# Kernel tuning notes

Measured on AMD Instinct MI355X. Metric: run time of the kernel, lower is better.

Reference implementation:

```python
import jax, jax.numpy as jnp
import numpy as np

B, C, S = 16, 128, 32          # batch, in_channel, img_size
HOLE_LO, HOLE_HI = 8, 24       # 16x16 hole where mask==1
HW = S * S
K = HW - (HOLE_HI - HOLE_LO) ** 2   # 768 context (unmasked) pixels per image
EPS = 1e-8                     # torch CosineSimilarity default eps


def setup_inputs() -> dict:
    key = jax.random.key(0)
    ks = jax.random.split(key, 3)
    x = jax.random.normal(ks[0], (B, C, S, S), dtype=jnp.float32)
    # mask: 1 inside the hole, 0 on the context region (fixed K per batch item)
    mask = jnp.zeros((B, 1, S, S), jnp.float32).at[:, :, HOLE_LO:HOLE_HI, HOLE_LO:HOLE_HI].set(1.0)
    # conv_regular_1: Conv2d(img_size**2 -> 256, k=5, pad=2); conv_regular_2: 256 -> 128
    W1 = jax.random.normal(ks[1], (256, HW, 5, 5), jnp.float32) / np.sqrt(HW * 25)
    b1 = jnp.zeros((256,), jnp.float32)
    W2 = jax.random.normal(ks[2], (128, 256, 5, 5), jnp.float32) / np.sqrt(256 * 25)
    b2 = jnp.zeros((128,), jnp.float32)
    return {"x": x, "mask": mask, "W1": W1, "b1": b1, "W2": W2, "b2": b2}


def _conv5x5(x, w, b):
    y = jax.lax.conv_general_dilated(x, w, window_strides=(1, 1),
                                     padding=[(2, 2), (2, 2)],
                                     dimension_numbers=("NCHW", "OIHW", "NCHW"))
    return y + b[None, :, None, None]


def reference(x, mask, W1, b1, W2, b2):
    # context (unmasked) pixel indices, row-major like torch.masked_select
    inv = (1.0 - mask[:, 0]) > 0.5                       # [B,S,S] bool
    idx = jax.vmap(lambda m: jnp.nonzero(m, size=K, fill_value=0)[0])(inv.reshape(B, HW))  # [B,K]
    xf = x.reshape(B, C, HW)                             # [B,C,HW]
    feat = jnp.take_along_axis(xf, idx[:, None, :], axis=2)  # [B,C,K] context features
    # cosine similarity over channel dim WITHOUT materializing [B,C,K,H,W] repeats
    dot = jnp.einsum("bck,bcp->bkp", feat, xf)           # [B,K,HW]
    nf = jnp.maximum(jnp.sqrt(jnp.sum(feat * feat, axis=1)), EPS)  # [B,K]
    nx = jnp.maximum(jnp.sqrt(jnp.sum(xf * xf, axis=1)), EPS)      # [B,HW]
    out = (dot / (nf[:, :, None] * nx[:, None, :])).reshape(B, K, S, S)
    out = out * mask                                     # keep hole region only
    pad = jnp.zeros((B, HW - K, S, S), out.dtype)
    out = jnp.concatenate([out, pad], axis=1)            # [B, HW, S, S]
    out = jax.nn.elu(_conv5x5(out, W1, b1))              # [B,256,S,S]
    out = jax.nn.elu(_conv5x5(out, W2, b2))              # [B,128,S,S]
    return out
```

## Files before the change

### kernel.cpp

```cpp
#include <hip/hip_runtime.h>
#include <hip/hip_fp16.h>
#include <math.h>


#define CC 128
#define HWN 1024
#define KK 768
#define PH 256

typedef _Float16 f16x8 __attribute__((ext_vector_type(8)));
typedef float f32x4 __attribute__((ext_vector_type(4)));

__device__ __forceinline__ int ctx_p(int k) {
    if (k < 256) return k;
    if (k < 512) {
        int r = (k - 256) >> 4, ci = (k - 256) & 15;
        int c = ci < 8 ? ci : ci + 16;
        return (8 + r) * 32 + c;
    }
    return k + 256;
}

__global__ __launch_bounds__(256) void kpre(const float* __restrict__ x,
                                            const float* __restrict__ W1, const float* __restrict__ W2,
                                            _Float16* __restrict__ cosT,
                                            _Float16* __restrict__ Wh1, _Float16* __restrict__ Wh2) {
    __shared__ float f[16][128];
    __shared__ float rfs[16];
    const int bid = blockIdx.x;
    const int t = threadIdx.x;
    if (bid < 768) {
        const int b = bid / 48;
        const int rem = bid - b * 48;
        const int hg = rem / 3, kch = rem - hg * 3;
        const int p16 = hg * 16;
        for (int s = t; s < 2048; s += 256) {
            int h = s >> 7, c = s & 127;
            int hp = p16 + h;
            f[h][c] = x[(b * CC + c) * HWN + (8 + (hp >> 4)) * 32 + 8 + (hp & 15)];
        }
        __syncthreads();
        {
            const int lane = t & 63, w = t >> 6;
#pragma unroll
            for (int i = 0; i < 4; ++i) {
                int h = w + i * 4;
                float v0 = f[h][lane], v1 = f[h][lane + 64];
                float pv = fmaf(v0, v0, v1 * v1);
#pragma unroll
                for (int m = 1; m < 64; m <<= 1) pv += __shfl_xor(pv, m, 64);
                if (lane == 0) rfs[h] = 1.0f / fmaxf(sqrtf(pv), 1e-8f);
            }
        }
        __syncthreads();
        const int k = kch * 256 + t;
        const int cp = ctx_p(k);
        const float* xp = x + b * CC * HWN + cp;
        float acc[16];
#pragma unroll
        for (int h = 0; h < 16; ++h) acc[h] = 0.f;
        float sk = 0.f;
        for (int c4 = 0; c4 < 128; c4 += 4) {
            float x0 = xp[(c4 + 0) * HWN];
            float x1 = xp[(c4 + 1) * HWN];
            float x2 = xp[(c4 + 2) * HWN];
            float x3 = xp[(c4 + 3) * HWN];
            sk = fmaf(x0, x0, sk); sk = fmaf(x1, x1, sk);
            sk = fmaf(x2, x2, sk); sk = fmaf(x3, x3, sk);
#pragma unroll
            for (int h = 0; h < 16; ++h) {
                float4 fv = *(const float4*)&f[h][c4];
                float a = acc[h];
                a = fmaf(fv.x, x0, a);
                a = fmaf(fv.y, x1, a);
                a = fmaf(fv.z, x2, a);
                a = fmaf(fv.w, x3, a);
                acc[h] = a;
            }
        }
        const float rk = 1.0f / fmaxf(sqrtf(sk), 1e-8f);
        _Float16* o = cosT + ((size_t)(b * PH + p16)) * KK + k;
#pragma unroll
        for (int h = 0; h < 16; ++h)
            o[(size_t)h * KK] = (_Float16)(acc[h] * rfs[h] * rk);
    } else {
        const int pid = bid - 768;
        if (pid < 768) {
            const int oc = pid & 255, kch = pid >> 8;
            const int k = kch * 256 + t;
            const float* wp = W1 + ((size_t)oc * HWN + k) * 25;
#pragma unroll
            for (int tap = 0; tap < 25; ++tap)
                Wh1[((size_t)(tap * 256 + oc)) * KK + k] = (_Float16)wp[tap];
        } else {
            const int oc = pid - 768;
            const float* wp = W2 + ((size_t)oc * 256 + t) * 25;
#pragma unroll
            for (int tap = 0; tap < 25; ++tap)
                Wh2[((size_t)(tap * 128 + oc)) * 256 + t] = (_Float16)wp[tap];
        }
    }
}

__global__ __launch_bounds__(512, 4) void kconv1m(const _Float16* __restrict__ cosT,
                                                  const _Float16* __restrict__ Wh1,
                                                  float* __restrict__ P, int kspan) {
    __shared__ __align__(16) char As[4 * 578 * 16];
    const int b = blockIdx.z, ks = blockIdx.x, nq = blockIdx.y;
    const int t = threadIdx.x;
    const int lane = t & 63, wid = t >> 6;
    const int mg = wid >> 1, ng = wid & 1;
    const int lm = lane & 15, kslot = lane >> 4;
    const int tile0 = (mg == 0) ? 0 : 6 * mg + 1;
    int pb[7];
#pragma unroll
    for (int mi = 0; mi < 7; ++mi) {
        int p = (tile0 + mi) * 16 + lm;
        if (p > 399) p = 399;
        pb[mi] = (kslot * 578 + (p / 20) * 24 + (p % 20)) * 16;
    }
    const f32x4 zero = {0.f, 0.f, 0.f, 0.f};
    f32x4 acc[7][2];
#pragma unroll
    for (int mi = 0; mi < 7; ++mi) { acc[mi][0] = zero; acc[mi][1] = zero; }

    const _Float16* Wb = Wh1 + (size_t)(nq * 64 + ng * 32 + lm) * KK + kslot * 8;

    const int kbeg = ks * kspan;
    for (int kc = kbeg; kc < kbeg + kspan; kc += 32) {
        __syncthreads();
        for (int s = t; s < 2304; s += 512) {
            int pos = s >> 2, slot = s & 3;
            int pu = pos / 24, pv = pos - pu * 24;
            int4 val = {0, 0, 0, 0};
            if (pu >= 4 && pu < 20 && pv >= 4 && pv < 20) {
                int hp = (pu - 4) * 16 + (pv - 4);
                val = *(const int4*)(cosT + ((size_t)(b * PH + hp)) * KK + kc + slot * 8);
            }
            *(int4*)(As + (slot * 578 + pos) * 16) = val;
        }
        __syncthreads();
        const _Float16* wkc = Wb + kc;
        f16x8 nb0 = *(const f16x8*)(wkc);
        f16x8 nb1 = *(const f16x8*)(wkc + 16 * KK);
#pragma unroll
        for (int tap = 0; tap < 25; ++tap) {
            const f16x8 b0 = nb0, b1 = nb1;
            if (tap < 24) {
                const _Float16* wn = wkc + (size_t)(tap + 1) * (256 * KK);
                nb0 = *(const f16x8*)(wn);
                nb1 = *(const f16x8*)(wn + 16 * KK);
            }
            const int off = ((tap / 5) * 24 + (tap % 5)) * 16;
#pragma unroll
            for (int mi = 0; mi < 6; ++mi) {
                f16x8 af = *(const f16x8*)(As + pb[mi] + off);
                acc[mi][0] = __builtin_amdgcn_mfma_f32_16x16x32_f16(af, b0, acc[mi][0], 0, 0, 0);
                acc[mi][1] = __builtin_amdgcn_mfma_f32_16x16x32_f16(af, b1, acc[mi][1], 0, 0, 0);
            }
            if (mg == 0) {
                f16x8 af = *(const f16x8*)(As + pb[6] + off);
                acc[6][0] = __builtin_amdgcn_mfma_f32_16x16x32_f16(af, b0, acc[6][0], 0, 0, 0);
                acc[6][1] = __builtin_amdgcn_mfma_f32_16x16x32_f16(af, b1, acc[6][1], 0, 0, 0);
            }
        }
    }
    float* Ps = P + ((size_t)((ks * 16 + b) * 4 + nq)) * 25600;
#pragma unroll
    for (int mi = 0; mi < 7; ++mi) {
        if (mi == 6 && mg != 0) continue;
#pragma unroll
        for (int j = 0; j < 2; ++j)
#pragma unroll
            for (int r = 0; r < 4; ++r) {
                int p = (tile0 + mi) * 16 + kslot * 4 + r;
                Ps[p * 64 + ng * 32 + j * 16 + lm] = acc[mi][j][r];
            }
    }
}

__global__ __launch_bounds__(256) void kreduce1(const float* __restrict__ P, const float* __restrict__ b1,
                                                _Float16* __restrict__ Y1T, int nks) {
    int i = blockIdx.x * 256 + threadIdx.x;
    int oc = i & 255;
    int nq = oc >> 6, ocl = oc & 63;
    int bp = i >> 8;
    int p = bp % 400, b = bp / 400;
    float s = 0.f;
    for (int ks = 0; ks < nks; ++ks)
        s += P[((size_t)((ks * 16 + b) * 4 + nq)) * 25600 + p * 64 + ocl];
    float y = s + b1[oc];
    y = y > 0.f ? y : expm1f(y);
    Y1T[((size_t)(b * 400 + p)) * 256 + oc] = (_Float16)y;
}

__global__ __launch_bounds__(512) void kconv2m(const _Float16* __restrict__ Y1T,
                                               const _Float16* __restrict__ Wh2,
                                               float* __restrict__ P) {
    __shared__ __align__(16) char As[4 * 786 * 16];
    const int b = blockIdx.z, ks = blockIdx.x, mh = blockIdx.y;
    const int t = threadIdx.x;
    const int lane = t & 63, wid = t >> 6;
    const int mg = wid >> 2, ng = wid & 3;
    const int lm = lane & 15, kslot = lane >> 4;
    const int ic0 = ks * 32;
    for (int s = t; s < 3136; s += 512) {
        int pos = s >> 2, slot = s & 3;
        int r = pos / 28, c = pos - r * 28;
        int4 val = {0, 0, 0, 0};
        if (r >= 4 && r < 24 && c >= 4 && c < 24)
            val = *(const int4*)(Y1T + ((size_t)(b * 400 + (r - 4) * 20 + (c - 4))) * 256 + ic0 + slot * 8);
        *(int4*)(As + (slot * 786 + pos) * 16) = val;
    }
    const int tile0 = mh * 18 + mg * 9;
    int pb[9];
#pragma unroll
    for (int mi = 0; mi < 9; ++mi) {
        int p = (tile0 + mi) * 16 + lm;
        pb[mi] = (kslot * 786 + (p / 24) * 28 + (p % 24)) * 16;
    }
    const f32x4 zero = {0.f, 0.f, 0.f, 0.f};
    f32x4 acc[9][2];
#pragma unroll
    for (int mi = 0; mi < 9; ++mi) { acc[mi][0] = zero; acc[mi][1] = zero; }
    const _Float16* Wb = Wh2 + (size_t)(ng * 32 + lm) * 256 + ic0 + kslot * 8;
    __syncthreads();
    f16x8 nb0 = *(const f16x8*)(Wb);
    f16x8 nb1 = *(const f16x8*)(Wb + 16 * 256);
#pragma unroll
    for (int tap = 0; tap < 25; ++tap) {
        const f16x8 b0 = nb0, b1 = nb1;
        if (tap < 24) {
            const _Float16* wn = Wb + (size_t)(tap + 1) * (128 * 256);
            nb0 = *(const f16x8*)(wn);
            nb1 = *(const f16x8*)(wn + 16 * 256);
        }
        const int off = ((tap / 5) * 28 + (tap % 5)) * 16;
#pragma unroll
        for (int mi = 0; mi < 9; ++mi) {
            f16x8 af = *(const f16x8*)(As + pb[mi] + off);
            acc[mi][0] = __builtin_amdgcn_mfma_f32_16x16x32_f16(af, b0, acc[mi][0], 0, 0, 0);
            acc[mi][1] = __builtin_amdgcn_mfma_f32_16x16x32_f16(af, b1, acc[mi][1], 0, 0, 0);
        }
    }
    float* Ps = P + ((size_t)((ks * 16 + b) * 2 + mh)) * 36864;
#pragma unroll
    for (int mi = 0; mi < 9; ++mi)
#pragma unroll
        for (int j = 0; j < 2; ++j)
#pragma unroll
            for (int r = 0; r < 4; ++r) {
                int p = (mg * 9 + mi) * 16 + kslot * 4 + r;
                Ps[p * 128 + ng * 32 + j * 16 + lm] = acc[mi][j][r];
            }
}

__global__ __launch_bounds__(256) void kreduce2(const float* __restrict__ P, const float* __restrict__ b2,
                                                float* __restrict__ out) {
    int i = blockIdx.x * 256 + threadIdx.x;
    int p = i & 1023;
    int oc = (i >> 10) & 127;
    int b = i >> 17;
    int u = p >> 5, v = p & 31;
    float y = 0.f;
    if (u >= 4 && u < 28 && v >= 4 && v < 28) {
        int pl = (u - 4) * 24 + (v - 4);
        int mh = pl >= 288 ? 1 : 0;
        int pll = pl - mh * 288;
        float s = 0.f;
#pragma unroll
        for (int ks = 0; ks < 8; ++ks)
            s += P[((size_t)((ks * 16 + b) * 2 + mh)) * 36864 + pll * 128 + oc];
        y = s + b2[oc];
        y = y > 0.f ? y : expm1f(y);
    }
    out[i] = y;
}

extern "C" void kernel_launch(void* const* d_in, const int* in_sizes, int n_in,
                              void* d_out, int out_size, void* d_ws, size_t ws_size,
                              hipStream_t stream) {
    const float* x  = (const float*)d_in[0];
    const float* W1 = (const float*)d_in[2];
    const float* b1 = (const float*)d_in[3];
    const float* W2 = (const float*)d_in[4];
    const float* b2 = (const float*)d_in[5];
    float* out = (float*)d_out;

    char* ws = (char*)d_ws;
    _Float16* cosT = (_Float16*)(ws + 0);
    _Float16* Wh1  = (_Float16*)(ws + 6291456);
    _Float16* Wh2  = (_Float16*)(ws + 16121856);
    _Float16* Y1T  = (_Float16*)(ws + 17760256);
    float*    P    = (float*)(ws + 21037056);

    const int nks = (ws_size >= 73465856ULL) ? 8 : 4;
    const int kspan = 768 / nks;

    kpre<<<1664, 256, 0, stream>>>(x, W1, W2, cosT, Wh1, Wh2);
    kconv1m<<<dim3(nks, 4, 16), 512, 0, stream>>>(cosT, Wh1, P, kspan);
    kreduce1<<<6400, 256, 0, stream>>>(P, b1, Y1T, nks);
    kconv2m<<<dim3(8, 2, 16), 512, 0, stream>>>(Y1T, Wh2, P);
    kreduce2<<<8192, 256, 0, stream>>>(P, b2, out);
}
```

Before: 271.0 us.

## Software-pipeline LDS and weight loads in conv MFMA loops; enlarge kpre tile

Both conv kernels now use double-buffered A fragments from LDS and triple-buffered B weight fragments from global memory, prefetching one or two taps ahead so MFMA issue overlaps load latency. The cosine-similarity precompute now handles 32 hole pixels per block instead of 16, which halves the number of times each context column of x is reread and changes the LDS load order. The cost is higher register pressure, with 32 accumulators in kpre and extra fragment buffers in the conv kernels, which could lower occupancy or cause spills under launch_bounds(512,4).

```diff
diff --git a/kernel.cpp b/kernel.cpp
--- a/kernel.cpp
+++ b/kernel.cpp
@@ -25,25 +25,25 @@
                                             const float* __restrict__ W1, const float* __restrict__ W2,
                                             _Float16* __restrict__ cosT,
                                             _Float16* __restrict__ Wh1, _Float16* __restrict__ Wh2) {
-    __shared__ float f[16][128];
-    __shared__ float rfs[16];
+    __shared__ float f[32][128];
+    __shared__ float rfs[32];
     const int bid = blockIdx.x;
     const int t = threadIdx.x;
-    if (bid < 768) {
-        const int b = bid / 48;
-        const int rem = bid - b * 48;
+    if (bid < 384) {
+        const int b = bid / 24;
+        const int rem = bid - b * 24;
         const int hg = rem / 3, kch = rem - hg * 3;
-        const int p16 = hg * 16;
-        for (int s = t; s < 2048; s += 256) {
-            int h = s >> 7, c = s & 127;
-            int hp = p16 + h;
+        const int p32 = hg * 32;
+        for (int s = t; s < 4096; s += 256) {
+            int h = s & 31, c = s >> 5;
+            int hp = p32 + h;
             f[h][c] = x[(b * CC + c) * HWN + (8 + (hp >> 4)) * 32 + 8 + (hp & 15)];
         }
         __syncthreads();
         {
             const int lane = t & 63, w = t >> 6;
 #pragma unroll
-            for (int i = 0; i < 4; ++i) {
+            for (int i = 0; i < 8; ++i) {
                 int h = w + i * 4;
                 float v0 = f[h][lane], v1 = f[h][lane + 64];
                 float pv = fmaf(v0, v0, v1 * v1);
@@ -56,9 +56,9 @@
         const int k = kch * 256 + t;
         const int cp = ctx_p(k);
         const float* xp = x + b * CC * HWN + cp;
-        float acc[16];
-#pragma unroll
-        for (int h = 0; h < 16; ++h) acc[h] = 0.f;
+        float acc[32];
+#pragma unroll
+        for (int h = 0; h < 32; ++h) acc[h] = 0.f;
         float sk = 0.f;
         for (int c4 = 0; c4 < 128; c4 += 4) {
             float x0 = xp[(c4 + 0) * HWN];
@@ -68,7 +68,7 @@
             sk = fmaf(x0, x0, sk); sk = fmaf(x1, x1, sk);
             sk = fmaf(x2, x2, sk); sk = fmaf(x3, x3, sk);
 #pragma unroll
-            for (int h = 0; h < 16; ++h) {
+            for (int h = 0; h < 32; ++h) {
                 float4 fv = *(const float4*)&f[h][c4];
                 float a = acc[h];
                 a = fmaf(fv.x, x0, a);
@@ -79,12 +79,12 @@
             }
         }
         const float rk = 1.0f / fmaxf(sqrtf(sk), 1e-8f);
-        _Float16* o = cosT + ((size_t)(b * PH + p16)) * KK + k;
-#pragma unroll
-        for (int h = 0; h < 16; ++h)
+        _Float16* o = cosT + ((size_t)(b * PH + p32)) * KK + k;
+#pragma unroll
+        for (int h = 0; h < 32; ++h)
             o[(size_t)h * KK] = (_Float16)(acc[h] * rfs[h] * rk);
     } else {
-        const int pid = bid - 768;
+        const int pid = bid - 384;
         if (pid < 768) {
             const int oc = pid & 255, kch = pid >> 8;
             const int k = kch * 256 + t;
@@ -101,6 +101,30 @@
         }
     }
 }
+
+#define LDA1(buf, tp) {                                                                   \
+        const int off_ = (((tp) / 5) * 24 + ((tp) % 5)) * 16;                             \
+        _Pragma("unroll")                                                                 \
+        for (int mi_ = 0; mi_ < 6; ++mi_)                                                 \
+            (buf)[mi_] = *(const f16x8*)(As + pb[mi_] + off_);                            \
+        if (mg == 0) (buf)[6] = *(const f16x8*)(As + pb[6] + off_);                       \
+    }
+#define LDB1(slot, tp) {                                                                  \
+        const _Float16* wn_ = wkc + (size_t)(tp) * (256 * KK);                            \
+        (slot)[0] = *(const f16x8*)(wn_);                                                 \
+        (slot)[1] = *(const f16x8*)(wn_ + 16 * KK);                                       \
+    }
+#define FMA1(buf, bb) {                                                                   \
+        _Pragma("unroll")                                                                 \
+        for (int mi_ = 0; mi_ < 6; ++mi_) {                                               \
+            acc[mi_][0] = __builtin_amdgcn_mfma_f32_16x16x32_f16((buf)[mi_], (bb)[0], acc[mi_][0], 0, 0, 0); \
+            acc[mi_][1] = __builtin_amdgcn_mfma_f32_16x16x32_f16((buf)[mi_], (bb)[1], acc[mi_][1], 0, 0, 0); \
+        }                                                                                 \
+        if (mg == 0) {                                                                    \
+            acc[6][0] = __builtin_amdgcn_mfma_f32_16x16x32_f16((buf)[6], (bb)[0], acc[6][0], 0, 0, 0); \
+            acc[6][1] = __builtin_amdgcn_mfma_f32_16x16x32_f16((buf)[6], (bb)[1], acc[6][1], 0, 0, 0); \
+        }                                                                                 \
+    }
 
 __global__ __launch_bounds__(512, 4) void kconv1m(const _Float16* __restrict__ cosT,
                                                   const _Float16* __restrict__ Wh1,
@@ -141,28 +165,16 @@
         }
         __syncthreads();
         const _Float16* wkc = Wb + kc;
-        f16x8 nb0 = *(const f16x8*)(wkc);
-        f16x8 nb1 = *(const f16x8*)(wkc + 16 * KK);
-#pragma unroll
-        for (int tap = 0; tap < 25; ++tap) {
-            const f16x8 b0 = nb0, b1 = nb1;
-            if (tap < 24) {
-                const _Float16* wn = wkc + (size_t)(tap + 1) * (256 * KK);
-                nb0 = *(const f16x8*)(wn);
-                nb1 = *(const f16x8*)(wn + 16 * KK);
-            }
-            const int off = ((tap / 5) * 24 + (tap % 5)) * 16;
-#pragma unroll
-            for (int mi = 0; mi < 6; ++mi) {
-                f16x8 af = *(const f16x8*)(As + pb[mi] + off);
-                acc[mi][0] = __builtin_amdgcn_mfma_f32_16x16x32_f16(af, b0, acc[mi][0], 0, 0, 0);
-                acc[mi][1] = __builtin_amdgcn_mfma_f32_16x16x32_f16(af, b1, acc[mi][1], 0, 0, 0);
-            }
-            if (mg == 0) {
-                f16x8 af = *(const f16x8*)(As + pb[6] + off);
-                acc[6][0] = __builtin_amdgcn_mfma_f32_16x16x32_f16(af, b0, acc[6][0], 0, 0, 0);
-                acc[6][1] = __builtin_amdgcn_mfma_f32_16x16x32_f16(af, b1, acc[6][1], 0, 0, 0);
-            }
+        f16x8 afq[2][7];
+        f16x8 bq[3][2];
+        LDA1(afq[0], 0);
+        LDB1(bq[0], 0);
+        LDB1(bq[1], 1);
+#pragma unroll
+        for (int tp = 0; tp < 25; ++tp) {
+            if (tp < 24) LDA1(afq[(tp + 1) & 1], tp + 1);
+            if (tp < 23) LDB1(bq[(tp + 2) % 3], tp + 2);
+            FMA1(afq[tp & 1], bq[tp % 3]);
         }
     }
     float* Ps = P + ((size_t)((ks * 16 + b) * 4 + nq)) * 25600;
@@ -193,6 +205,25 @@
     y = y > 0.f ? y : expm1f(y);
     Y1T[((size_t)(b * 400 + p)) * 256 + oc] = (_Float16)y;
 }
+
+#define LDA2(buf, tp) {                                                                   \
+        const int off_ = (((tp) / 5) * 28 + ((tp) % 5)) * 16;                             \
+        _Pragma("unroll")                                                                 \
+        for (int mi_ = 0; mi_ < 9; ++mi_)                                                 \
+            (buf)[mi_] = *(const f16x8*)(As + pb[mi_] + off_);                            \
+    }
+#define LDB2(slot, tp) {                                                                  \
+        const _Float16* wn_ = Wb + (size_t)(tp) * (128 * 256);                            \
+        (slot)[0] = *(const f16x8*)(wn_);                                                 \
+        (slot)[1] = *(const f16x8*)(wn_ + 16 * 256);                                      \
+    }
+#define FMA2(buf, bb) {                                                                   \
+        _Pragma("unroll")                                                                 \
+        for (int mi_ = 0; mi_ < 9; ++mi_) {                                               \
+            acc[mi_][0] = __builtin_amdgcn_mfma_f32_16x16x32_f16((buf)[mi_], (bb)[0], acc[mi_][0], 0, 0, 0); \
+            acc[mi_][1] = __builtin_amdgcn_mfma_f32_16x16x32_f16((buf)[mi_], (bb)[1], acc[mi_][1], 0, 0, 0); \
+        }                                                                                 \
+    }
 
 __global__ __launch_bounds__(512) void kconv2m(const _Float16* __restrict__ Y1T,
                                                const _Float16* __restrict__ Wh2,
@@ -225,23 +256,16 @@
     for (int mi = 0; mi < 9; ++mi) { acc[mi][0] = zero; acc[mi][1] = zero; }
     const _Float16* Wb = Wh2 + (size_t)(ng * 32 + lm) * 256 + ic0 + kslot * 8;
     __syncthreads();
-    f16x8 nb0 = *(const f16x8*)(Wb);
-    f16x8 nb1 = *(const f16x8*)(Wb + 16 * 256);
-#pragma unroll
-    for (int tap = 0; tap < 25; ++tap) {
-        const f16x8 b0 = nb0, b1 = nb1;
-        if (tap < 24) {
-            const _Float16* wn = Wb + (size_t)(tap + 1) * (128 * 256);
-            nb0 = *(const f16x8*)(wn);
-            nb1 = *(const f16x8*)(wn + 16 * 256);
-        }
-        const int off = ((tap / 5) * 28 + (tap % 5)) * 16;
-#pragma unroll
-        for (int mi = 0; mi < 9; ++mi) {
-            f16x8 af = *(const f16x8*)(As + pb[mi] + off);
-            acc[mi][0] = __builtin_amdgcn_mfma_f32_16x16x32_f16(af, b0, acc[mi][0], 0, 0, 0);
-            acc[mi][1] = __builtin_amdgcn_mfma_f32_16x16x32_f16(af, b1, acc[mi][1], 0, 0, 0);
-        }
+    f16x8 afq[2][9];
+    f16x8 bq[3][2];
+    LDA2(afq[0], 0);
+    LDB2(bq[0], 0);
+    LDB2(bq[1], 1);
+#pragma unroll
+    for (int tp = 0; tp < 25; ++tp) {
+        if (tp < 24) LDA2(afq[(tp + 1) & 1], tp + 1);
+        if (tp < 23) LDB2(bq[(tp + 2) % 3], tp + 2);
+        FMA2(afq[tp & 1], bq[tp % 3]);
     }
     float* Ps = P + ((size_t)((ks * 16 + b) * 2 + mh)) * 36864;
 #pragma unroll
@@ -297,7 +321,7 @@
     const int nks = (ws_size >= 73465856ULL) ? 8 : 4;
     const int kspan = 768 / nks;
 
-    kpre<<<1664, 256, 0, stream>>>(x, W1, W2, cosT, Wh1, Wh2);
+    kpre<<<1280, 256, 0, stream>>>(x, W1, W2, cosT, Wh1, Wh2);
     kconv1m<<<dim3(nks, 4, 16), 512, 0, stream>>>(cosT, Wh1, P, kspan);
     kreduce1<<<6400, 256, 0, stream>>>(P, b1, Y1T, nks);
     kconv2m<<<dim3(8, 2, 16), 512, 0, stream>>>(Y1T, Wh2, P);
```

Result: slower. 381.6 us (+40.8%).
